# Kernel tuning notes

Hardware: AMD Instinct MI355X
Metric: run time of the kernel (lower is better)

Reference implementation:

```python
import jax, jax.numpy as jnp
import numpy as np

B, T, C = 1024, 8192, 2   # batch, seq_len, num_labels
MS = 128                  # max_sentences
RANK_W, PRUNE_W = 1.0, 0.5


def setup_inputs() -> dict:
    key = jax.random.key(0)
    k1, k2, k3, k4, k5, k6 = jax.random.split(key, 6)
    ranking_logits = jax.random.normal(k1, (B,), dtype=jnp.float32)
    ranking_labels = jax.random.uniform(k2, (B,), dtype=jnp.float32)
    pruning_logits = jax.random.normal(k3, (B, T, C), dtype=jnp.float32)
    pruning_labels = jax.random.randint(k4, (B, MS), 0, C, dtype=jnp.int64)
    # Contiguous sentence boundaries: sorted cut points covering [0, T].
    cuts = jnp.sort(jax.random.randint(k5, (B, MS + 1), 0, T + 1, dtype=jnp.int64), axis=1)
    cuts = cuts.at[:, 0].set(0).at[:, -1].set(T)
    starts = cuts[:, :-1]  # [B, MS]
    ends = cuts[:, 1:]     # [B, MS]
    # Mark a random suffix of sentences invalid (-1), like padded sentence slots.
    n_valid = jax.random.randint(k6, (B, 1), 96, MS + 1, dtype=jnp.int64)
    keep = jnp.arange(MS, dtype=jnp.int64)[None, :] < n_valid  # [B, MS]
    starts = jnp.where(keep, starts, -1)
    ends = jnp.where(keep, ends, -1)
    boundaries = jnp.stack([starts, ends], axis=-1)  # [B, MS, 2]
    return {
        "ranking_logits": ranking_logits,
        "ranking_labels": ranking_labels,
        "pruning_logits": pruning_logits,
        "pruning_labels": pruning_labels,
        "boundaries": boundaries,
    }


def _bce_with_logits(x, y):
    # BCEWithLogitsLoss(mean): y*softplus(-x) + (1-y)*softplus(x)
    return jnp.mean(y * jax.nn.softplus(-x) + (1.0 - y) * jax.nn.softplus(x))


def _sentence_level_loss(logits, labels, boundaries):
    # logits [B,T,C], labels [B,MS] int, boundaries [B,MS,2] int.
    # Mean-pool tokens in [start, end) per sentence via prefix sums (segment reduce).
    b, t, c = logits.shape
    cp = jnp.concatenate(
        [jnp.zeros((b, 1, c), dtype=logits.dtype), jnp.cumsum(logits, axis=1)], axis=1
    )  # [B, T+1, C]
    starts, ends = boundaries[..., 0], boundaries[..., 1]  # [B, MS]
    valid = starts != -1
    s = jnp.clip(starts, 0, t)
    e = jnp.clip(ends, 0, t)
    bidx = jnp.arange(b)[:, None]
    seg_sum = cp[bidx, e] - cp[bidx, s]                     # [B, MS, C]
    length = (e - s).astype(logits.dtype)[..., None]        # [B, MS, 1]
    pooled = jnp.where(length > 0, seg_sum / jnp.maximum(length, 1.0), 0.0)
    logp = jax.nn.log_softmax(pooled, axis=-1)              # [B, MS, C]
    nll = -jnp.take_along_axis(logp, labels[..., None], axis=-1)[..., 0]  # [B, MS]
    vf = valid.astype(logits.dtype)
    count = jnp.sum(vf)
    return jnp.where(count > 0, jnp.sum(nll * vf) / jnp.maximum(count, 1.0), 0.0)


def reference(ranking_logits, ranking_labels, pruning_logits, pruning_labels, boundaries):
    ranking_loss = _bce_with_logits(ranking_logits, ranking_labels)
    pruning_loss = _sentence_level_loss(pruning_logits, pruning_labels, boundaries)
    return RANK_W * ranking_loss + PRUNE_W * pruning_loss
```

## Files before the change

### kernel.cpp

```cpp
#include <hip/hip_runtime.h>

constexpr int B   = 1024;
constexpr int T   = 8192;
constexpr int MS  = 128;
constexpr int NF4 = T / 2;

__device__ __forceinline__ int pidx(int k) { return k + (k >> 4); }

__global__ __launch_bounds__(256, 4) void seg_loss_kernel(
    const float* __restrict__ rlogits,
    const float* __restrict__ rlabels,
    const float* __restrict__ logits,
    const int*   __restrict__ labels,
    const int*   __restrict__ bnd,
    float4*      __restrict__ partial)
{
    const int b    = blockIdx.x;
    const int tid  = threadIdx.x;
    const int lane = tid & 63;
    const int wave = tid >> 6;
    const float* row = logits + (size_t)b * T * 2;

    __shared__ float2 E2[NF4 + (NF4 >> 4) + 2];
    __shared__ float  wtot0[4], wtot1[4];
    __shared__ float  rn[4], rc[4];

    int s_ = -1, e_ = -1, lab_ = 0;
    if (tid < MS) {
        const size_t bm = (size_t)b * MS + tid;
        s_   = bnd[bm * 2 + 0];
        e_   = bnd[bm * 2 + 1];
        lab_ = labels[bm];
    }
    float bce_b = 0.f;
    if (tid == 0) {
        const float x = rlogits[b];
        const float y = rlabels[b];
        const float t = log1pf(expf(-fabsf(x)));
        bce_b = y * (fmaxf(-x, 0.f) + t) + (1.f - y) * (fmaxf(x, 0.f) + t);
    }

    float4 v[16];
    {
        const float4* p = reinterpret_cast<const float4*>(row) + (size_t)tid * 16;
        #pragma unroll
        for (int j = 0; j < 16; ++j) v[j] = p[j];
    }
    __builtin_amdgcn_sched_barrier(0);
    float ex0 = 0.f, ex1 = 0.f;
    #pragma unroll
    for (int j = 0; j < 16; ++j) {
        ex0 += v[j].x + v[j].z;
        ex1 += v[j].y + v[j].w;
    }

    float x0 = ex0, x1 = ex1;
    #pragma unroll
    for (int off = 1; off < 64; off <<= 1) {
        float y0 = __shfl_up(x0, off, 64);
        float y1 = __shfl_up(x1, off, 64);
        if (lane >= off) { x0 += y0; x1 += y1; }
    }
    if (lane == 63) { wtot0[wave] = x0; wtot1[wave] = x1; }
    __syncthreads();
    float pre0 = 0.f, pre1 = 0.f;
    #pragma unroll
    for (int w = 0; w < 3; ++w) {
        if (wave > w) { pre0 += wtot0[w]; pre1 += wtot1[w]; }
    }
    const float incl0 = x0 + pre0,    incl1 = x1 + pre1;
    float run0 = incl0 - ex0, run1 = incl1 - ex1;
    #pragma unroll
    for (int j = 0; j < 16; ++j) {
        E2[17 * tid + j] = make_float2(run0, run1);
        run0 += v[j].x + v[j].z;
        run1 += v[j].y + v[j].w;
    }
    if (tid == 255) E2[pidx(NF4)] = make_float2(run0, run1);
    __syncthreads();

    float nll = 0.f, cnt = 0.f;
    if (tid < MS && s_ != -1) {
        const int sc = min(max(s_, 0), T);
        const int ec = min(max(e_, 0), T);
        const int cs = sc >> 1;
        const int ce = ec >> 1;

        const float2 Ps = E2[pidx(cs)];
        const float2 Pe = E2[pidx(ce)];
        float q0 = Pe.x - Ps.x;
        float q1 = Pe.y - Ps.y;
        if (sc & 1) {
            float2 u = *reinterpret_cast<const float2*>(row + (size_t)(sc - 1) * 2);
            q0 -= u.x; q1 -= u.y;
        }
        if (ec & 1) {
            float2 u = *reinterpret_cast<const float2*>(row + (size_t)(ec - 1) * 2);
            q0 += u.x; q1 += u.y;
        }

        const int len = ec - sc;
        float p0 = 0.f, p1 = 0.f;
        if (len > 0) {
            const float inv = 1.0f / (float)len;
            p0 = q0 * inv;
            p1 = q1 * inv;
        }
        const float mx  = fmaxf(p0, p1);
        const float lse = mx + logf(expf(p0 - mx) + expf(p1 - mx));
        nll = lse - ((lab_ == 0) ? p0 : p1);
        cnt = 1.0f;
    }

    #pragma unroll
    for (int off = 32; off > 0; off >>= 1) {
        nll += __shfl_down(nll, off, 64);
        cnt += __shfl_down(cnt, off, 64);
    }
    if (lane == 0) { rn[wave] = nll; rc[wave] = cnt; }
    __syncthreads();
    if (tid == 0) {
        partial[b] = make_float4(rn[0] + rn[1] + rn[2] + rn[3],
                                 rc[0] + rc[1] + rc[2] + rc[3],
                                 bce_b, 0.f);
    }
}

__global__ __launch_bounds__(256) void finalize_kernel(
    const float4* __restrict__ partial,
    float*        __restrict__ out)
{
    const int tid  = threadIdx.x;
    const int lane = tid & 63;
    const int wave = tid >> 6;

    float nll = 0.f, cnt = 0.f, bce = 0.f;
    #pragma unroll
    for (int i = 0; i < 4; ++i) {
        const float4 p = partial[tid + i * 256];
        nll += p.x; cnt += p.y; bce += p.z;
    }

    #pragma unroll
    for (int off = 32; off > 0; off >>= 1) {
        nll += __shfl_down(nll, off, 64);
        cnt += __shfl_down(cnt, off, 64);
        bce += __shfl_down(bce, off, 64);
    }
    __shared__ float sn[4], sc[4], sb[4];
    if (lane == 0) { sn[wave] = nll; sc[wave] = cnt; sb[wave] = bce; }
    __syncthreads();
    if (tid == 0) {
        const float tn = sn[0] + sn[1] + sn[2] + sn[3];
        const float tc = sc[0] + sc[1] + sc[2] + sc[3];
        const float tb = sb[0] + sb[1] + sb[2] + sb[3];
        const float rank  = tb / (float)B;
        const float prune = (tc > 0.f) ? (tn / tc) : 0.f;
        out[0] = 1.0f * rank + 0.5f * prune;
    }
}

extern "C" void kernel_launch(void* const* d_in, const int* in_sizes, int n_in,
                              void* d_out, int out_size, void* d_ws, size_t ws_size,
                              hipStream_t stream) {
    const float* rlogits = (const float*)d_in[0];
    const float* rlabels = (const float*)d_in[1];
    const float* plogits = (const float*)d_in[2];
    const int*   plabels = (const int*)  d_in[3];
    const int*   bnd     = (const int*)  d_in[4];

    float*  out     = (float*)d_out;
    float4* partial = (float4*)d_ws;

    seg_loss_kernel<<<B, 256, 0, stream>>>(rlogits, rlabels, plogits,
                                           plabels, bnd, partial);
    finalize_kernel<<<1, 256, 0, stream>>>(partial, out);
}
```

Before: 19.71 us.

## Skip loading tokens beyond the last valid sentence end and use 512-thread blocks

Each block first reduces the largest clamped end boundary over its valid sentences. Threads whose token chunk lies entirely past that point skip their global loads and contribute zeros to the prefix scan. The block also grows to 512 threads, each owning 8 float2 pairs instead of 16, which pre-adds token pairs on load and cuts register use per thread. The aim is to avoid reading logits that no valid sentence uses and to keep more loads in flight. The cost is an extra reduction and barrier before the loads, plus longer wave-level scan and reduction overhead.

Result: no change. 19.89 us (+1.0%).

```diff
diff --git a/kernel.cpp b/kernel.cpp
--- a/kernel.cpp
+++ b/kernel.cpp
@@ -7,7 +7,7 @@
 
 __device__ __forceinline__ int pidx(int k) { return k + (k >> 4); }
 
-__global__ __launch_bounds__(256, 4) void seg_loss_kernel(
+__global__ __launch_bounds__(512, 8) void seg_loss_kernel(
     const float* __restrict__ rlogits,
     const float* __restrict__ rlabels,
     const float* __restrict__ logits,
@@ -22,8 +22,9 @@
     const float* row = logits + (size_t)b * T * 2;
 
     __shared__ float2 E2[NF4 + (NF4 >> 4) + 2];
-    __shared__ float  wtot0[4], wtot1[4];
-    __shared__ float  rn[4], rc[4];
+    __shared__ float  wtot0[8], wtot1[8];
+    __shared__ float  rn[8], rc[8];
+    __shared__ int    wemax[2];
 
     int s_ = -1, e_ = -1, lab_ = 0;
     if (tid < MS) {
@@ -39,20 +40,34 @@
         const float t = log1pf(expf(-fabsf(x)));
         bce_b = y * (fmaxf(-x, 0.f) + t) + (1.f - y) * (fmaxf(x, 0.f) + t);
     }
+    int emax = (tid < MS && s_ != -1) ? min(max(e_, 0), T) : 0;
+    #pragma unroll
+    for (int off = 32; off > 0; off >>= 1)
+        emax = max(emax, __shfl_down(emax, off, 64));
+    if (wave < 2 && lane == 0) wemax[wave] = emax;
+    __syncthreads();
+    const int max_e = max(wemax[0], wemax[1]);
 
-    float4 v[16];
-    {
-        const float4* p = reinterpret_cast<const float4*>(row) + (size_t)tid * 16;
+    float2 pair[8];
+    const int chunk_lo = tid << 4;
+    if (chunk_lo < max_e) {
+        const float4* p = reinterpret_cast<const float4*>(row) + (size_t)tid * 8;
         #pragma unroll
-        for (int j = 0; j < 16; ++j) v[j] = p[j];
+        for (int g = 0; g < 2; ++g) {
+            float4 w0 = p[g * 4 + 0], w1 = p[g * 4 + 1];
+            float4 w2 = p[g * 4 + 2], w3 = p[g * 4 + 3];
+            pair[g * 4 + 0] = make_float2(w0.x + w0.z, w0.y + w0.w);
+            pair[g * 4 + 1] = make_float2(w1.x + w1.z, w1.y + w1.w);
+            pair[g * 4 + 2] = make_float2(w2.x + w2.z, w2.y + w2.w);
+            pair[g * 4 + 3] = make_float2(w3.x + w3.z, w3.y + w3.w);
+        }
+    } else {
+        #pragma unroll
+        for (int j = 0; j < 8; ++j) pair[j] = make_float2(0.f, 0.f);
     }
-    __builtin_amdgcn_sched_barrier(0);
     float ex0 = 0.f, ex1 = 0.f;
     #pragma unroll
-    for (int j = 0; j < 16; ++j) {
-        ex0 += v[j].x + v[j].z;
-        ex1 += v[j].y + v[j].w;
-    }
+    for (int j = 0; j < 8; ++j) { ex0 += pair[j].x; ex1 += pair[j].y; }
 
     float x0 = ex0, x1 = ex1;
     #pragma unroll
@@ -65,18 +80,18 @@
     __syncthreads();
     float pre0 = 0.f, pre1 = 0.f;
     #pragma unroll
-    for (int w = 0; w < 3; ++w) {
+    for (int w = 0; w < 7; ++w) {
         if (wave > w) { pre0 += wtot0[w]; pre1 += wtot1[w]; }
     }
-    const float incl0 = x0 + pre0,    incl1 = x1 + pre1;
-    float run0 = incl0 - ex0, run1 = incl1 - ex1;
+    float run0 = x0 + pre0 - ex0, run1 = x1 + pre1 - ex1;
     #pragma unroll
-    for (int j = 0; j < 16; ++j) {
-        E2[17 * tid + j] = make_float2(run0, run1);
-        run0 += v[j].x + v[j].z;
-        run1 += v[j].y + v[j].w;
+    for (int j = 0; j < 8; ++j) {
+        const int k = 8 * tid + j;
+        E2[pidx(k)] = make_float2(run0, run1);
+        run0 += pair[j].x;
+        run1 += pair[j].y;
     }
-    if (tid == 255) E2[pidx(NF4)] = make_float2(run0, run1);
+    if (tid == 511) E2[pidx(NF4)] = make_float2(run0, run1);
     __syncthreads();
 
     float nll = 0.f, cnt = 0.f;
@@ -120,9 +135,10 @@
     if (lane == 0) { rn[wave] = nll; rc[wave] = cnt; }
     __syncthreads();
     if (tid == 0) {
-        partial[b] = make_float4(rn[0] + rn[1] + rn[2] + rn[3],
-                                 rc[0] + rc[1] + rc[2] + rc[3],
-                                 bce_b, 0.f);
+        float tn = 0.f, tc = 0.f;
+        #pragma unroll
+        for (int w = 0; w < 8; ++w) { tn += rn[w]; tc += rc[w]; }
+        partial[b] = make_float4(tn, tc, bce_b, 0.f);
     }
 }
 
@@ -172,7 +188,7 @@
     float*  out     = (float*)d_out;
     float4* partial = (float4*)d_ws;
 
-    seg_loss_kernel<<<B, 256, 0, stream>>>(rlogits, rlabels, plogits,
+    seg_loss_kernel<<<B, 512, 0, stream>>>(rlogits, rlabels, plogits,
                                            plabels, bnd, partial);
     finalize_kernel<<<1, 256, 0, stream>>>(partial, out);
 }
```

## Replace per-block partials with fixed-point atomic accumulation and hoist logits load

Applied to the files above, without the earlier changes.

Each block now quantizes its NLL sum and BCE term to 64-bit fixed point and adds them, along with its count, into three global atomic counters. This replaces writing per-block partials that a second kernel had to reduce. The finalize kernel shrinks to a single thread that converts the counters back, but a memset is added to the stream to clear them. The logits loads are also moved before the boundary and label loads and the sched_barrier is dropped, so memory issue can start earlier.

Result: slower. 60.41 us (+206.6%).

```diff
diff --git a/kernel.cpp b/kernel.cpp
--- a/kernel.cpp
+++ b/kernel.cpp
@@ -7,13 +7,15 @@
 
 __device__ __forceinline__ int pidx(int k) { return k + (k >> 4); }
 
+constexpr double FXP = 4294967296.0;
+
 __global__ __launch_bounds__(256, 4) void seg_loss_kernel(
     const float* __restrict__ rlogits,
     const float* __restrict__ rlabels,
     const float* __restrict__ logits,
     const int*   __restrict__ labels,
     const int*   __restrict__ bnd,
-    float4*      __restrict__ partial)
+    unsigned long long* __restrict__ acc)
 {
     const int b    = blockIdx.x;
     const int tid  = threadIdx.x;
@@ -24,6 +26,13 @@
     __shared__ float2 E2[NF4 + (NF4 >> 4) + 2];
     __shared__ float  wtot0[4], wtot1[4];
     __shared__ float  rn[4], rc[4];
+
+    float4 v[16];
+    {
+        const float4* p = reinterpret_cast<const float4*>(row) + (size_t)tid * 16;
+        #pragma unroll
+        for (int j = 0; j < 16; ++j) v[j] = p[j];
+    }
 
     int s_ = -1, e_ = -1, lab_ = 0;
     if (tid < MS) {
@@ -40,13 +49,6 @@
         bce_b = y * (fmaxf(-x, 0.f) + t) + (1.f - y) * (fmaxf(x, 0.f) + t);
     }
 
-    float4 v[16];
-    {
-        const float4* p = reinterpret_cast<const float4*>(row) + (size_t)tid * 16;
-        #pragma unroll
-        for (int j = 0; j < 16; ++j) v[j] = p[j];
-    }
-    __builtin_amdgcn_sched_barrier(0);
     float ex0 = 0.f, ex1 = 0.f;
     #pragma unroll
     for (int j = 0; j < 16; ++j) {
@@ -68,7 +70,7 @@
     for (int w = 0; w < 3; ++w) {
         if (wave > w) { pre0 += wtot0[w]; pre1 += wtot1[w]; }
     }
-    const float incl0 = x0 + pre0,    incl1 = x1 + pre1;
+    const float incl0 = x0 + pre0, incl1 = x1 + pre1;
     float run0 = incl0 - ex0, run1 = incl1 - ex1;
     #pragma unroll
     for (int j = 0; j < 16; ++j) {
@@ -120,43 +122,27 @@
     if (lane == 0) { rn[wave] = nll; rc[wave] = cnt; }
     __syncthreads();
     if (tid == 0) {
-        partial[b] = make_float4(rn[0] + rn[1] + rn[2] + rn[3],
-                                 rc[0] + rc[1] + rc[2] + rc[3],
-                                 bce_b, 0.f);
+        const float tn = rn[0] + rn[1] + rn[2] + rn[3];
+        const float tc = rc[0] + rc[1] + rc[2] + rc[3];
+        const long long qn = (long long)((double)tn * FXP +
+                                         ((double)tn >= 0.0 ? 0.5 : -0.5));
+        const long long qb = (long long)((double)bce_b * FXP + 0.5);
+        atomicAdd(&acc[0], (unsigned long long)qn);
+        atomicAdd(&acc[1], (unsigned long long)(long long)tc);
+        atomicAdd(&acc[2], (unsigned long long)qb);
     }
 }
 
-__global__ __launch_bounds__(256) void finalize_kernel(
-    const float4* __restrict__ partial,
-    float*        __restrict__ out)
+__global__ void finalize_kernel(const unsigned long long* __restrict__ acc,
+                                float* __restrict__ out)
 {
-    const int tid  = threadIdx.x;
-    const int lane = tid & 63;
-    const int wave = tid >> 6;
-
-    float nll = 0.f, cnt = 0.f, bce = 0.f;
-    #pragma unroll
-    for (int i = 0; i < 4; ++i) {
-        const float4 p = partial[tid + i * 256];
-        nll += p.x; cnt += p.y; bce += p.z;
-    }
-
-    #pragma unroll
-    for (int off = 32; off > 0; off >>= 1) {
-        nll += __shfl_down(nll, off, 64);
-        cnt += __shfl_down(cnt, off, 64);
-        bce += __shfl_down(bce, off, 64);
-    }
-    __shared__ float sn[4], sc[4], sb[4];
-    if (lane == 0) { sn[wave] = nll; sc[wave] = cnt; sb[wave] = bce; }
-    __syncthreads();
-    if (tid == 0) {
-        const float tn = sn[0] + sn[1] + sn[2] + sn[3];
-        const float tc = sc[0] + sc[1] + sc[2] + sc[3];
-        const float tb = sb[0] + sb[1] + sb[2] + sb[3];
-        const float rank  = tb / (float)B;
-        const float prune = (tc > 0.f) ? (tn / tc) : 0.f;
-        out[0] = 1.0f * rank + 0.5f * prune;
+    if (threadIdx.x == 0) {
+        const double nll = (double)(long long)acc[0] / FXP;
+        const double cnt = (double)(long long)acc[1];
+        const double bce = (double)(long long)acc[2] / FXP;
+        const double rank  = bce / (double)B;
+        const double prune = (cnt > 0.0) ? (nll / cnt) : 0.0;
+        out[0] = (float)(rank + 0.5 * prune);
     }
 }
 
@@ -169,10 +155,12 @@
     const int*   plabels = (const int*)  d_in[3];
     const int*   bnd     = (const int*)  d_in[4];
 
-    float*  out     = (float*)d_out;
-    float4* partial = (float4*)d_ws;
+    float* out = (float*)d_out;
+    unsigned long long* acc = (unsigned long long*)d_ws;
+
+    hipMemsetAsync(acc, 0, 3 * sizeof(unsigned long long), stream);
 
     seg_loss_kernel<<<B, 256, 0, stream>>>(rlogits, rlabels, plogits,
-                                           plabels, bnd, partial);
-    finalize_kernel<<<1, 256, 0, stream>>>(partial, out);
+                                           plabels, bnd, acc);
+    finalize_kernel<<<1, 64, 0, stream>>>(acc, out);
 }
```
